# Kernel optimization log

Hardware: AMD Instinct MI355X
Metric: run time of the kernel (lower is better)

The kernel has to match this reference:

```python
import jax, jax.numpy as jnp
import numpy as np

B, N, C = 128, 197, 768   # batch, tokens (14*14 + cls), embed dim
H = 12                    # attention heads, head_dim = 64
OUT = 32                  # hard-coded mlp out_features
CH_H = 14                 # channel-attention heads
CN = 196                  # channel-attention token dim (14*14)
MLP_HID = int(C * 4.0)    # 3072
CMLP_HID = int(OUT * 4.0) # 128
EPS = 1e-5


def _ln(x, g, b):
    m = x.mean(-1, keepdims=True)
    v = ((x - m) ** 2).mean(-1, keepdims=True)
    return (x - m) * jax.lax.rsqrt(v + EPS) * g + b


def setup_inputs() -> dict:
    key = jax.random.key(0)
    ks = jax.random.split(key, 24)
    W = lambda k, sh: (jax.random.normal(k, sh, jnp.float32) * 0.02)
    return {
        "x": jax.random.normal(ks[0], (B, N, C), jnp.float32),
        # block 1: norm1 + token attention
        "g1": jnp.ones((C,), jnp.float32), "b1": jnp.zeros((C,), jnp.float32),
        "w_qkv": W(ks[1], (3 * C, C)),                     # qkv_bias=False
        "w_proj": W(ks[2], (C, C)), "b_proj": jnp.zeros((C,), jnp.float32),
        # block 2: norm2 + mlp (768 -> 3072 -> 32), NOT residual
        "g2": jnp.ones((C,), jnp.float32), "b2": jnp.zeros((C,), jnp.float32),
        "w_fc1": W(ks[3], (MLP_HID, C)), "b_fc1": jnp.zeros((MLP_HID,), jnp.float32),
        "w_fc2": W(ks[4], (OUT, MLP_HID)), "b_fc2": jnp.zeros((OUT,), jnp.float32),
        # block 3: norm3 + channel attention (over 196 spatial positions)
        "g3": jnp.ones((OUT,), jnp.float32), "b3": jnp.zeros((OUT,), jnp.float32),
        "w_cqkv": W(ks[5], (3 * CN, CN)),                  # qkv_bias=False
        "w_cproj": W(ks[6], (CN, CN)), "b_cproj": jnp.zeros((CN,), jnp.float32),
        # block 4: norm4 + channel mlp (32 -> 128 -> 32)
        "g4": jnp.ones((OUT,), jnp.float32), "b4": jnp.zeros((OUT,), jnp.float32),
        "w_cfc1": W(ks[7], (CMLP_HID, OUT)), "b_cfc1": jnp.zeros((CMLP_HID,), jnp.float32),
        "w_cfc2": W(ks[8], (OUT, CMLP_HID)), "b_cfc2": jnp.zeros((OUT,), jnp.float32),
    }


def reference(x, g1, b1, w_qkv, w_proj, b_proj,
              g2, b2, w_fc1, b_fc1, w_fc2, b_fc2,
              g3, b3, w_cqkv, w_cproj, b_cproj,
              g4, b4, w_cfc1, b_cfc1, w_cfc2, b_cfc2):
    Bz, Nn, Cc = x.shape
    hd = Cc // H  # 64

    # --- token attention (residual) ---
    h = _ln(x, g1, b1)
    qkv = (h @ w_qkv.T).reshape(Bz, Nn, 3, H, hd).transpose(2, 0, 3, 1, 4)
    q, k, v = qkv[0], qkv[1], qkv[2]                       # [B,H,N,hd]
    a = jax.nn.softmax(jnp.einsum('bhqd,bhkd->bhqk', q, k) * (hd ** -0.5), axis=-1)
    o = jnp.einsum('bhqk,bhkd->bhqd', a, v).transpose(0, 2, 1, 3).reshape(Bz, Nn, Cc)
    x = x + (o @ w_proj.T + b_proj)

    # --- mlp 768->3072->32, NO residual (matches original forward) ---
    h = _ln(x, g2, b2)
    x = jax.nn.gelu(h @ w_fc1.T + b_fc1, approximate=False) @ w_fc2.T + b_fc2  # [B,N,32]

    # --- channel attention (residual); N==197 path, no interleave averaging ---
    h = _ln(x, g3, b3)
    cls = h[:, :1, :]                                      # [B,1,32]
    t = h[:, 1:, :].transpose(0, 2, 1)                     # [B,32,196]
    chd = CN // CH_H  # 14
    cqkv = (t @ w_cqkv.T).reshape(Bz, OUT, 3, CH_H, chd).transpose(2, 0, 3, 1, 4)
    cq, ck, cv = cqkv[0], cqkv[1], cqkv[2]                 # [B,14,32,14]
    ca = jax.nn.softmax(jnp.einsum('bhqd,bhkd->bhqk', cq, ck) * (chd ** -0.5), axis=-1)
    co = jnp.einsum('bhqk,bhkd->bhqd', ca, cv).transpose(0, 2, 1, 3).reshape(Bz, OUT, CN)
    co = co @ w_cproj.T + b_cproj                          # [B,32,196]
    x = x + jnp.concatenate([cls, co.transpose(0, 2, 1)], axis=1)

    # --- channel mlp 32->128->32 (residual) ---
    h = _ln(x, g4, b4)
    x = x + (jax.nn.gelu(h @ w_cfc1.T + b_cfc1, approximate=False) @ w_cfc2.T + b_cfc2)
    return x
```

## Files before the change

### kernel.cpp

```cpp
#include <hip/hip_runtime.h>
#include <hip/hip_bf16.h>

typedef unsigned short u16;
typedef __hip_bfloat16 bf16;
typedef __attribute__((ext_vector_type(8))) short bf16x8;
typedef __attribute__((ext_vector_type(4))) float f32x4;

#define B_   128
#define N_   197
#define C_   768
#define H_   12
#define HD_  64
#define T_   (B_*N_)
#define MH_  3072
#define OUT_ 32
#define CN_  196
#define CHH_ 14
#define KP_  224
#define CSZ_ (B_*CHH_*32*14)

__device__ __forceinline__ float bfu2f(u16 x){ union{unsigned u; float f;} v; v.u=((unsigned)x)<<16; return v.f; }
__device__ __forceinline__ bf16  f2bf(float f){ return __float2bfloat16(f); }
__device__ __forceinline__ u16   f2bfu(float f){ union{bf16 h; u16 u;} c; c.h=__float2bfloat16(f); return c.u; }
__device__ __forceinline__ float gelu_f(float x){ return 0.5f*x*(1.0f+erff(x*0.70710678118654752f)); }

__device__ __forceinline__ void gl_lds16(const u16* g, u16* l){
  __builtin_amdgcn_global_load_lds((const __attribute__((address_space(1))) void*)g,
                                   (__attribute__((address_space(3))) void*)l, 16, 0, 0);
}

__global__ __launch_bounds__(256) void write_code_kernel(float* out, int n, float code){
  int i = blockIdx.x*256 + threadIdx.x;
  if (i < n) out[i] = code;
}

template<bool F32IN>
__global__ __launch_bounds__(256) void ln768_kernel(const void* __restrict__ xv,
    const float* __restrict__ g, const float* __restrict__ b, bf16* __restrict__ out)
{
  int row = blockIdx.x;
  int tid = threadIdx.x;
  float v0, v1, v2;
  if (F32IN){
    const float* xr = (const float*)xv + (size_t)row*C_;
    v0 = xr[tid]; v1 = xr[tid+256]; v2 = xr[tid+512];
  } else {
    const u16* xr = (const u16*)xv + (size_t)row*C_;
    v0 = bfu2f(xr[tid]); v1 = bfu2f(xr[tid+256]); v2 = bfu2f(xr[tid+512]);
  }
  __shared__ float red[4];
  int lane = tid & 63, wave = tid >> 6;
  float s = v0+v1+v2;
  #pragma unroll
  for (int off=32; off>0; off>>=1) s += __shfl_xor(s, off);
  if (lane==0) red[wave]=s;
  __syncthreads();
  float mean = (red[0]+red[1]+red[2]+red[3]) * (1.0f/C_);
  float d0=v0-mean, d1=v1-mean, d2=v2-mean;
  float q = d0*d0+d1*d1+d2*d2;
  #pragma unroll
  for (int off=32; off>0; off>>=1) q += __shfl_xor(q, off);
  __syncthreads();
  if (lane==0) red[wave]=q;
  __syncthreads();
  float var = (red[0]+red[1]+red[2]+red[3]) * (1.0f/C_);
  float r = rsqrtf(var + 1e-5f);
  bf16* orow = out + (size_t)row*C_;
  orow[tid]     = f2bf(d0*r*g[tid]     + b[tid]);
  orow[tid+256] = f2bf(d1*r*g[tid+256] + b[tid+256]);
  orow[tid+512] = f2bf(d2*r*g[tid+512] + b[tid+512]);
}

__global__ __launch_bounds__(256) void ln32_kernel(const float* __restrict__ x,
    const float* __restrict__ g, const float* __restrict__ b, float* __restrict__ out)
{
  int i = blockIdx.x*256 + threadIdx.x;
  int c = i & 31;
  float v = x[i];
  float s = v;
  #pragma unroll
  for (int off=16; off>0; off>>=1) s += __shfl_xor(s, off, 32);
  float mean = s * (1.0f/32);
  float d = v - mean;
  float q = d*d;
  #pragma unroll
  for (int off=16; off>0; off>>=1) q += __shfl_xor(q, off, 32);
  float r = rsqrtf(q*(1.0f/32) + 1e-5f);
  out[i] = d*r*g[c] + b[c];
}

__global__ __launch_bounds__(256) void packw_bf16(const float* __restrict__ w,
    u16* __restrict__ dst, int n)
{
  int i = (blockIdx.x*256 + threadIdx.x)*4;
  if (i >= n) return;
  float4 v = *(const float4*)(w + i);
  ushort4 o; o.x=f2bfu(v.x); o.y=f2bfu(v.y); o.z=f2bfu(v.z); o.w=f2bfu(v.w);
  *(ushort4*)(dst + i) = o;
}

__global__ __launch_bounds__(256) void init_x3_kernel(const float* __restrict__ bias,
    float* __restrict__ x3)
{
  int i = blockIdx.x*256 + threadIdx.x;
  x3[i] = bias[i & 31];
}

template<int MODE, bool WB16>
__global__ __launch_bounds__(256) void gemm128(
    const u16* __restrict__ A, const void* __restrict__ Wsrc,
    const float* __restrict__ bias, const float* __restrict__ resid,
    bf16* __restrict__ outb,
    bf16* __restrict__ q_out, bf16* __restrict__ k_out, bf16* __restrict__ v_out,
    int Nn, int K)
{
  __shared__ __align__(16) u16 As[2][128*32];
  __shared__ __align__(16) u16 Bs[2][128*32];
  const int tid  = threadIdx.x;
  const int wave = tid >> 6, lane = tid & 63;
  const int quad = lane >> 4, l16 = lane & 15;
  const int wr = wave >> 1, wc = wave & 1;
  const int m0 = blockIdx.y * 128;
  const int n0 = blockIdx.x * 128;
  const int rs = tid >> 2;
  const int kc = (tid & 3) << 3;

  const u16* aA0 = A + (size_t)(m0 + rs)*K + kc;
  const u16* aA1 = aA0 + (size_t)64*K;
  const u16*  wB0 = WB16 ? ((const u16*)Wsrc + (size_t)(n0 + rs)*K + kc) : nullptr;
  const float* wF0 = WB16 ? nullptr : ((const float*)Wsrc + (size_t)(n0 + rs)*K + kc);

  f32x4 acc[4][4] = {};

  auto STAGE = [&](int buf, int k0){
    u16* AsW = As[buf] + (size_t)wave*512;
    u16* BsW = Bs[buf] + (size_t)wave*512;
    gl_lds16(aA0 + k0, AsW);
    gl_lds16(aA1 + k0, AsW + 2048);
    if (WB16){
      gl_lds16(wB0 + k0, BsW);
      gl_lds16(wB0 + (size_t)64*K + k0, BsW + 2048);
    } else {
      float4 w0 = *(const float4*)(wF0 + k0);
      float4 w1 = *(const float4*)(wF0 + k0 + 4);
      const float* wF1 = wF0 + (size_t)64*K;
      float4 w2 = *(const float4*)(wF1 + k0);
      float4 w3 = *(const float4*)(wF1 + k0 + 4);
      ushort4 b0; b0.x=f2bfu(w0.x); b0.y=f2bfu(w0.y); b0.z=f2bfu(w0.z); b0.w=f2bfu(w0.w);
      ushort4 b1; b1.x=f2bfu(w1.x); b1.y=f2bfu(w1.y); b1.z=f2bfu(w1.z); b1.w=f2bfu(w1.w);
      ushort4 b2; b2.x=f2bfu(w2.x); b2.y=f2bfu(w2.y); b2.z=f2bfu(w2.z); b2.w=f2bfu(w2.w);
      ushort4 b3; b3.x=f2bfu(w3.x); b3.y=f2bfu(w3.y); b3.z=f2bfu(w3.z); b3.w=f2bfu(w3.w);
      *(ushort4*)&Bs[buf][rs*32 + kc]        = b0;
      *(ushort4*)&Bs[buf][rs*32 + kc + 4]    = b1;
      *(ushort4*)&Bs[buf][(rs+64)*32 + kc]   = b2;
      *(ushort4*)&Bs[buf][(rs+64)*32 + kc+4] = b3;
    }
  };

  STAGE(0, 0);
  __syncthreads();
  int cur = 0;

  for (int k0 = 0; k0 < K; k0 += 32){
    if (k0 + 32 < K) STAGE(cur^1, k0 + 32);
    bf16x8 af[4], bfr[4];
    #pragma unroll
    for (int i=0;i<4;i++) af[i]  = *(const bf16x8*)&As[cur][(wr*64 + i*16 + l16)*32 + quad*8];
    #pragma unroll
    for (int j=0;j<4;j++) bfr[j] = *(const bf16x8*)&Bs[cur][(wc*64 + j*16 + l16)*32 + quad*8];
    #pragma unroll
    for (int i=0;i<4;i++)
      #pragma unroll
      for (int j=0;j<4;j++)
        acc[i][j] = __builtin_amdgcn_mfma_f32_16x16x32_bf16(af[i], bfr[j], acc[i][j], 0, 0, 0);
    __syncthreads();
    cur ^= 1;
  }

  #pragma unroll
  for (int i=0;i<4;i++){
    #pragma unroll
    for (int j=0;j<4;j++){
      #pragma unroll
      for (int r=0;r<4;r++){
        int m = m0 + wr*64 + i*16 + quad*4 + r;
        int c = n0 + wc*64 + j*16 + l16;
        float v = acc[i][j][r];
        if (MODE==0){
          int bb = m / N_;
          int n  = m - bb*N_;
          int sec = c / C_;
          int rem = c - sec*C_;
          int hh  = rem >> 6;
          int d   = rem & 63;
          bf16* dst = (sec==0) ? q_out : (sec==1) ? k_out : v_out;
          dst[(((size_t)bb*H_ + hh)*N_ + n)*HD_ + d] = f2bf(v);
        } else if (MODE==1){
          size_t idx = (size_t)m*Nn + c;
          outb[idx] = f2bf(v + bias[c] + resid[idx]);
        } else {
          outb[(size_t)m*Nn + c] = f2bf(gelu_f(v + bias[c]));
        }
      }
    }
  }
}

template<int MODE, bool WB16>
__global__ __launch_bounds__(256) void gemm_mfma(
    const u16* __restrict__ A, const void* __restrict__ Wsrc,
    const float* __restrict__ bias, const float* __restrict__ resid,
    bf16* __restrict__ outb, float* __restrict__ outf,
    bf16* __restrict__ q_out, bf16* __restrict__ k_out, bf16* __restrict__ v_out,
    int M, int Nn, int K, int wld, int astride)
{
  __shared__ __align__(16) u16 As[64][32];
  __shared__ __align__(16) u16 Bs[64][32];
  const int tid  = threadIdx.x;
  const int wave = tid >> 6, lane = tid & 63;
  const int quad = lane >> 4, l16 = lane & 15;
  const int m0 = blockIdx.x * 64;
  const int n0 = (MODE==6) ? 0 : blockIdx.y * 64;
  const int kst = (MODE==6) ? blockIdx.y * K : 0;
  const int rs = tid >> 2;
  const int kc = (tid & 3) << 3;
  const u16* arow = A + (size_t)(m0 + rs)*astride + kst + kc;
  const bool wvalid = (n0 + rs) < Nn;

  f32x4 acc[4] = {};

  for (int k0 = 0; k0 < K; k0 += 32){
    *(uint4*)&As[rs][kc] = *(const uint4*)(arow + k0);
    if (WB16){
      const u16* wrow = (const u16*)Wsrc + (size_t)(n0 + rs)*wld + kst + kc;
      uint4 wv = make_uint4(0u,0u,0u,0u);
      if (wvalid) wv = *(const uint4*)(wrow + k0);
      *(uint4*)&Bs[rs][kc] = wv;
    } else {
      const float* wrow = (const float*)Wsrc + (size_t)(n0 + rs)*wld + kst + kc;
      float4 w0 = make_float4(0.f,0.f,0.f,0.f), w1 = w0;
      if (wvalid){ w0 = *(const float4*)(wrow + k0); w1 = *(const float4*)(wrow + k0 + 4); }
      ushort4 b0; b0.x=f2bfu(w0.x); b0.y=f2bfu(w0.y); b0.z=f2bfu(w0.z); b0.w=f2bfu(w0.w);
      ushort4 b1; b1.x=f2bfu(w1.x); b1.y=f2bfu(w1.y); b1.z=f2bfu(w1.z); b1.w=f2bfu(w1.w);
      *(ushort4*)&Bs[rs][kc]   = b0;
      *(ushort4*)&Bs[rs][kc+4] = b1;
    }
    __syncthreads();
    bf16x8 af = *(const bf16x8*)&As[wave*16 + l16][quad*8];
    #pragma unroll
    for (int nb=0; nb<4; nb++){
      bf16x8 bfr = *(const bf16x8*)&Bs[nb*16 + l16][quad*8];
      acc[nb] = __builtin_amdgcn_mfma_f32_16x16x32_bf16(af, bfr, acc[nb], 0, 0, 0);
    }
    __syncthreads();
  }

  #pragma unroll
  for (int nb=0; nb<4; nb++){
    #pragma unroll
    for (int r=0; r<4; r++){
      int m = m0 + wave*16 + quad*4 + r;
      int c = n0 + nb*16 + l16;
      float v = acc[nb][r];
      if (MODE==3){
        if (c < Nn) outf[(size_t)m*Nn + c] = v + bias[c];
      } else if (MODE==4){
        if (c < Nn) outf[(size_t)m*Nn + c] += v;
      } else if (MODE==6){
        if (c < Nn) atomicAdd(&outf[(size_t)m*Nn + c], v);
      } else if (MODE==5){
        if (c < Nn){
          int bb = m >> 5, oo = m & 31;
          int sec = c / CN_;
          int rem = c - sec*CN_;
          int hh  = rem / 14;
          int d   = rem - hh*14;
          outf[(size_t)sec*CSZ_ + (((size_t)bb*CHH_ + hh)*32 + oo)*14 + d] = v;
        }
      }
    }
  }
}

__global__ __launch_bounds__(256) void attn_kernel(const u16* __restrict__ q,
    const u16* __restrict__ k, const u16* __restrict__ v, bf16* __restrict__ o)
{
  __shared__ __align__(16) u16 VtS[64*208];
  __shared__ __align__(16) u16 PsS[4*16*208];
  int bid = blockIdx.x;
  int bh = bid >> 1, sh = bid & 1;
  int b = bh / H_, hh = bh - b*H_;
  int tid = threadIdx.x, wave = tid >> 6, lane = tid & 63;
  int quad = lane >> 4, l16 = lane & 15;
  const u16* qb = q + (size_t)bh*N_*HD_;
  const u16* kb = k + (size_t)bh*N_*HD_;
  const u16* vb = v + (size_t)bh*N_*HD_;
  for (int idx = tid; idx < N_*HD_; idx += 256){
    int j = idx >> 6, d = idx & 63;
    VtS[(d*208 + j) ^ ((d&7)<<3)] = vb[idx];
  }
  for (int idx = tid; idx < 64*11; idx += 256){
    int d = idx / 11, j = 197 + (idx - d*11);
    VtS[(d*208 + j) ^ ((d&7)<<3)] = 0;
  }
  __syncthreads();

  u16* PsW = PsS + wave*16*208;
  const int gbeg = sh ? 7 : 0;
  const int gend = sh ? 13 : 7;
  const float LOG2E = 1.4426950408889634f;

  for (int g = gbeg + wave; g < gend; g += 4){
    int r0 = g*16;
    int qrow = r0 + l16;
    int qr = (qrow < N_) ? qrow : 0;
    bf16x8 aq0 = *(const bf16x8*)(qb + (size_t)qr*HD_ + quad*8);
    bf16x8 aq1 = *(const bf16x8*)(qb + (size_t)qr*HD_ + 32 + quad*8);
    f32x4 s[13];
    __builtin_amdgcn_s_setprio(1);
    #pragma unroll
    for (int nb = 0; nb < 13; nb++){
      int krow = nb*16 + l16;
      int kr = (krow < N_) ? krow : 0;
      bf16x8 bk0 = *(const bf16x8*)(kb + (size_t)kr*HD_ + quad*8);
      bf16x8 bk1 = *(const bf16x8*)(kb + (size_t)kr*HD_ + 32 + quad*8);
      f32x4 t = {};
      t = __builtin_amdgcn_mfma_f32_16x16x32_bf16(aq0, bk0, t, 0, 0, 0);
      t = __builtin_amdgcn_mfma_f32_16x16x32_bf16(aq1, bk1, t, 0, 0, 0);
      s[nb] = t;
    }
    __builtin_amdgcn_s_setprio(0);
    #pragma unroll
    for (int nb = 0; nb < 13; nb++){
      bool colok = (nb*16 + l16) < N_;
      #pragma unroll
      for (int r = 0; r < 4; r++)
        s[nb][r] = colok ? s[nb][r]*(0.125f*LOG2E) : -1e30f;
    }
    #pragma unroll
    for (int r = 0; r < 4; r++){
      float m01 = fmaxf(s[0][r], s[1][r]),  m23 = fmaxf(s[2][r], s[3][r]);
      float m45 = fmaxf(s[4][r], s[5][r]),  m67 = fmaxf(s[6][r], s[7][r]);
      float m89 = fmaxf(s[8][r], s[9][r]),  mab = fmaxf(s[10][r], s[11][r]);
      float m = fmaxf(fmaxf(fmaxf(m01,m23), fmaxf(m45,m67)),
                      fmaxf(fmaxf(m89,mab), s[12][r]));
      m = fmaxf(m, __shfl_xor(m, 1));
      m = fmaxf(m, __shfl_xor(m, 2));
      m = fmaxf(m, __shfl_xor(m, 4));
      m = fmaxf(m, __shfl_xor(m, 8));
      float p[13];
      #pragma unroll
      for (int nb = 0; nb < 13; nb++){
        p[nb] = __builtin_amdgcn_exp2f(s[nb][r] - m);
        s[nb][r] = p[nb];
      }
      float t01=p[0]+p[1], t23=p[2]+p[3], t45=p[4]+p[5], t67=p[6]+p[7];
      float t89=p[8]+p[9], tab=p[10]+p[11];
      float su = ((t01+t23)+(t45+t67)) + ((t89+tab)+p[12]);
      su += __shfl_xor(su, 1);
      su += __shfl_xor(su, 2);
      su += __shfl_xor(su, 4);
      su += __shfl_xor(su, 8);
      float inv = 1.0f/su;
      #pragma unroll
      for (int nb = 0; nb < 13; nb++) s[nb][r] *= inv;
    }
    #pragma unroll
    for (int nb = 0; nb < 13; nb++)
      #pragma unroll
      for (int r = 0; r < 4; r++){
        int row = quad*4 + r;
        PsW[(row*208 + nb*16 + l16) ^ ((row&7)<<3)] = f2bfu(s[nb][r]);
      }
    __threadfence_block();
    f32x4 oa[4] = {};
    __builtin_amdgcn_s_setprio(1);
    #pragma unroll
    for (int ks = 0; ks < 7; ks++){
      int col = ks*32 + quad*8;
      bool ok = (col < 208);
      int ccol = ok ? col : 0;
      bf16x8 ap = *(const bf16x8*)&PsW[(l16*208 + ccol) ^ ((l16&7)<<3)];
      if (!ok) ap = (bf16x8){0,0,0,0,0,0,0,0};
      #pragma unroll
      for (int nd = 0; nd < 4; nd++){
        bf16x8 bv = *(const bf16x8*)&VtS[((nd*16 + l16)*208 + ccol) ^ ((l16&7)<<3)];
        oa[nd] = __builtin_amdgcn_mfma_f32_16x16x32_bf16(ap, bv, oa[nd], 0, 0, 0);
      }
    }
    __builtin_amdgcn_s_setprio(0);
    #pragma unroll
    for (int nd = 0; nd < 4; nd++)
      #pragma unroll
      for (int r = 0; r < 4; r++){
        int qi = r0 + quad*4 + r;
        if (qi < N_)
          o[((size_t)b*N_ + qi)*C_ + hh*HD_ + nd*16 + l16] = f2bf(oa[nd][r]);
      }
    __threadfence_block();
  }
}

__global__ __launch_bounds__(256) void pack_tall_kernel(const float* __restrict__ h3,
    u16* __restrict__ tall)
{
  int idx = blockIdx.x*256 + threadIdx.x;
  if (idx >= 4096*KP_) return;
  int row = idx / KP_, kk = idx - row*KP_;
  int b = row >> 5, oo = row & 31;
  float v = (kk < CN_) ? h3[((size_t)b*N_ + 1 + kk)*32 + oo] : 0.f;
  tall[idx] = f2bfu(v);
}

__global__ __launch_bounds__(256) void pack_w_kernel(const float* __restrict__ w,
    u16* __restrict__ dst, int rows, int kreal)
{
  int idx = blockIdx.x*256 + threadIdx.x;
  if (idx >= rows*KP_) return;
  int r = idx / KP_, kk = idx - r*KP_;
  dst[idx] = (kk < kreal) ? f2bfu(w[(size_t)r*kreal + kk]) : (u16)0;
}

__global__ __launch_bounds__(256) void pack_co_kernel(const float* __restrict__ co,
    u16* __restrict__ dst)
{
  int idx = blockIdx.x*256 + threadIdx.x;
  if (idx >= 4096*KP_) return;
  int row = idx / KP_, kk = idx - row*KP_;
  dst[idx] = (kk < CN_) ? f2bfu(co[(size_t)row*CN_ + kk]) : (u16)0;
}

__global__ __launch_bounds__(64) void cattn_kernel(const float* __restrict__ cq,
    const float* __restrict__ ck, const float* __restrict__ cv, float* __restrict__ co)
{
  __shared__ __align__(16) float qs[32*15], ks_[32*15], vs[32*15], ps[32*34];
  int bh = blockIdx.x;
  int b  = bh / CHH_;
  int hh = bh - b*CHH_;
  int lane = threadIdx.x;
  const float* qb = cq + (size_t)bh*448;
  const float* kb = ck + (size_t)bh*448;
  const float* vb = cv + (size_t)bh*448;
  for (int idx=lane; idx<448; idx+=64){
    int o = idx/14, d = idx - o*14;
    qs[o*15+d] = qb[idx]; ks_[o*15+d] = kb[idx]; vs[o*15+d] = vb[idx];
  }
  __syncthreads();
  int o = lane & 31, half = lane >> 5;
  const float scale = 0.2672612419124244f;
  float sc[16]; float mx = -1e30f;
  #pragma unroll
  for (int jj=0; jj<16; jj++){
    int j = half*16 + jj;
    float a = 0.f;
    #pragma unroll
    for (int d=0; d<14; d++) a += qs[o*15+d]*ks_[j*15+d];
    sc[jj] = a*scale;
    mx = fmaxf(mx, sc[jj]);
  }
  mx = fmaxf(mx, __shfl_xor(mx, 32));
  float sum = 0.f;
  #pragma unroll
  for (int jj=0; jj<16; jj++){ sc[jj] = __expf(sc[jj]-mx); sum += sc[jj]; }
  sum += __shfl_xor(sum, 32);
  float inv = 1.0f/sum;
  #pragma unroll
  for (int jj=0; jj<16; jj++) ps[o*34 + half*16 + jj] = sc[jj]*inv;
  __syncthreads();
  #pragma unroll
  for (int dd=0; dd<7; dd++){
    int d = half*7 + dd;
    float acc = 0.f;
    #pragma unroll
    for (int j=0; j<32; j++) acc += ps[o*34+j]*vs[j*15+d];
    co[((size_t)b*32 + o)*CN_ + hh*14 + d] = acc;
  }
}

__global__ __launch_bounds__(256) void concat_add_kernel(const float* __restrict__ x3,
    const float* __restrict__ h3, const float* __restrict__ co2, float* __restrict__ x4)
{
  int i = blockIdx.x*256 + threadIdx.x;
  int c = i & 31;
  int row = i >> 5;
  int b = row / N_;
  int r = row - b*N_;
  float add = (r==0) ? h3[i] : co2[((size_t)b*32 + c)*CN_ + (r-1)];
  x4[i] = x3[i] + add;
}

__global__ __launch_bounds__(256) void cfc1_kernel(const float* __restrict__ h4,
    const float* __restrict__ w, const float* __restrict__ bias, float* __restrict__ chid)
{
  int idx = blockIdx.x*256 + threadIdx.x;
  int m = idx >> 7, j = idx & 127;
  const float* hr = h4 + (size_t)m*32;
  const float* wr = w + (size_t)j*32;
  float acc = bias[j];
  #pragma unroll
  for (int kk=0; kk<32; kk++) acc += hr[kk]*wr[kk];
  chid[idx] = gelu_f(acc);
}

__global__ __launch_bounds__(256) void cfc2_kernel(const float* __restrict__ chid,
    const float* __restrict__ w, const float* __restrict__ bias,
    const float* __restrict__ x4, float* __restrict__ out)
{
  int idx = blockIdx.x*256 + threadIdx.x;
  int m = idx >> 5, j = idx & 31;
  const float* cr = chid + (size_t)m*128;
  const float* wr = w + (size_t)j*128;
  float acc = bias[j];
  #pragma unroll
  for (int kk=0; kk<128; kk++) acc += cr[kk]*wr[kk];
  out[idx] = x4[idx] + acc;
}

extern "C" void kernel_launch(void* const* d_in, const int* in_sizes, int n_in,
                              void* d_out, int out_size, void* d_ws, size_t ws_size,
                              hipStream_t stream)
{
  const int NIN = 23;
  static const int dsz[NIN] = {19365888,768,768,1769472,589824,768,768,768,2359296,
                               3072,98304,32,32,32,115248,38416,196,32,32,4096,128,4096,32};
  static const int a2d[NIN] = {2,7,13,18,20,22,16,9,11,5,1,6,12,17,19,21,15,14,8,10,4,3,0};

  float* dout = (float*)d_out;
  int ogrid = (out_size + 255)/256;

  const float* in[NIN];
  bool dict_ok = (n_in == NIN);
  if (dict_ok) for (int i=0;i<NIN;i++) if (in_sizes[i] != dsz[i]) { dict_ok=false; break; }
  if (dict_ok){
    for (int i=0;i<NIN;i++) in[i] = (const float*)d_in[i];
  } else {
    bool alpha_ok = (n_in == NIN);
    if (alpha_ok) for (int i=0;i<NIN;i++) if (in_sizes[i] != dsz[a2d[i]]) { alpha_ok=false; break; }
    if (alpha_ok){
      for (int i=0;i<NIN;i++) in[a2d[i]] = (const float*)d_in[i];
    } else {
      write_code_kernel<<<ogrid, 256, 0, stream>>>(dout, out_size, 5000.f + (float)n_in);
      return;
    }
  }

  const float* x      = in[0];
  const float* g1     = in[1];
  const float* b1     = in[2];
  const float* w_qkv  = in[3];
  const float* w_proj = in[4];
  const float* b_proj = in[5];
  const float* g2     = in[6];
  const float* b2     = in[7];
  const float* w_fc1  = in[8];
  const float* b_fc1  = in[9];
  const float* w_fc2  = in[10];
  const float* b_fc2  = in[11];
  const float* g3     = in[12];
  const float* b3     = in[13];
  const float* w_cqkv = in[14];
  const float* w_cproj= in[15];
  const float* b_cproj= in[16];
  const float* g4     = in[17];
  const float* b4     = in[18];
  const float* w_cfc1 = in[19];
  const float* b_cfc1 = in[20];
  const float* w_cfc2 = in[21];
  const float* b_cfc2 = in[22];

  char* ws = (char*)d_ws;
  const size_t TC2 = (size_t)T_*C_*2;
  const size_t NEED = 4*TC2 + 4096;
  if (ws_size < NEED){
    write_code_kernel<<<ogrid, 256, 0, stream>>>(dout, out_size,
        7000.f + (float)(ws_size >> 20));
    return;
  }

  bf16* h_buf   = (bf16*)(ws);
  bf16* o_buf   = (bf16*)(ws);
  bf16* q_buf   = (bf16*)(ws + TC2);
  bf16* k_buf   = (bf16*)(ws + 2*TC2);
  bf16* v_buf   = (bf16*)(ws + 3*TC2);
  bf16* x2_buf  = (bf16*)(ws + TC2);
  bf16* hidh    = (bf16*)(ws + 2*TC2);
  float* x3     = (float*)(ws + TC2);
  char* sm = ws + 2*TC2;
  float* h3  = (float*)sm; sm += (size_t)T_*32*4;
  float* cq  = (float*)sm; sm += (size_t)CSZ_*4;
  float* ck  = (float*)sm; sm += (size_t)CSZ_*4;
  float* cv  = (float*)sm; sm += (size_t)CSZ_*4;
  float* co  = (float*)sm; sm += (size_t)B_*32*CN_*4;
  float* co2 = (float*)sm; sm += (size_t)B_*32*CN_*4;
  float* x4  = (float*)sm; sm += (size_t)T_*32*4;
  float* h4  = (float*)sm; sm += (size_t)T_*32*4;
  float* chid = (float*)sm;
  u16* tall  = (u16*)(ws);
  u16* wcq_b = (u16*)(ws + 2*1024*1024);
  u16* co_b  = (u16*)(ws + 3*1024*1024);
  u16* wcp_b = (u16*)(ws + 5*1024*1024);

  u16* wqkv_b  = (u16*)(ws + 4*TC2 + 4096);
  u16* wproj_b = wqkv_b  + (size_t)2304*C_;
  u16* wfc1_b  = wproj_b + (size_t)C_*C_;
  const size_t WPACK = ((size_t)2304*C_ + (size_t)C_*C_ + (size_t)MH_*C_)*2;
  const bool packed = (ws_size >= NEED + WPACK);

  if (packed){
    packw_bf16<<<(2304*C_/4+255)/256, 256, 0, stream>>>(w_qkv,  wqkv_b,  2304*C_);
    packw_bf16<<<(C_*C_/4+255)/256,  256, 0, stream>>>(w_proj, wproj_b, C_*C_);
    packw_bf16<<<(MH_*C_/4+255)/256, 256, 0, stream>>>(w_fc1,  wfc1_b,  MH_*C_);
  }

  ln768_kernel<true><<<T_, 256, 0, stream>>>(x, g1, b1, h_buf);
  if (packed)
    gemm128<0,true><<<dim3(2304/128, T_/128), 256, 0, stream>>>((const u16*)h_buf,
        wqkv_b, nullptr, nullptr, nullptr, q_buf, k_buf, v_buf, 2304, C_);
  else
    gemm128<0,false><<<dim3(2304/128, T_/128), 256, 0, stream>>>((const u16*)h_buf,
        w_qkv, nullptr, nullptr, nullptr, q_buf, k_buf, v_buf, 2304, C_);
  attn_kernel<<<B_*H_*2, 256, 0, stream>>>((const u16*)q_buf, (const u16*)k_buf,
      (const u16*)v_buf, o_buf);
  if (packed)
    gemm128<1,true><<<dim3(C_/128, T_/128), 256, 0, stream>>>((const u16*)o_buf,
        wproj_b, b_proj, x, x2_buf, nullptr, nullptr, nullptr, C_, C_);
  else
    gemm128<1,false><<<dim3(C_/128, T_/128), 256, 0, stream>>>((const u16*)o_buf,
        w_proj, b_proj, x, x2_buf, nullptr, nullptr, nullptr, C_, C_);
  ln768_kernel<false><<<T_, 256, 0, stream>>>(x2_buf, g2, b2, h_buf);
  init_x3_kernel<<<(T_*32)/256, 256, 0, stream>>>(b_fc2, x3);
  for (int half=0; half<2; half++){
    if (packed)
      gemm128<2,true><<<dim3(1536/128, T_/128), 256, 0, stream>>>((const u16*)h_buf,
          wfc1_b + (size_t)half*1536*C_, b_fc1 + half*1536, nullptr,
          hidh, nullptr, nullptr, nullptr, 1536, C_);
    else
      gemm128<2,false><<<dim3(1536/128, T_/128), 256, 0, stream>>>((const u16*)h_buf,
          w_fc1 + (size_t)half*1536*C_, b_fc1 + half*1536, nullptr,
          hidh, nullptr, nullptr, nullptr, 1536, C_);
    gemm_mfma<6,false><<<dim3(T_/64, 4), 256, 0, stream>>>((const u16*)hidh,
        w_fc2 + (size_t)half*1536, nullptr, nullptr, nullptr, x3,
        nullptr, nullptr, nullptr, T_, OUT_, 384, MH_, 1536);
  }
  ln32_kernel<<<(T_*32)/256, 256, 0, stream>>>(x3, g3, b3, h3);
  pack_tall_kernel<<<(4096*KP_+255)/256, 256, 0, stream>>>(h3, tall);
  pack_w_kernel<<<(588*KP_+255)/256, 256, 0, stream>>>(w_cqkv, wcq_b, 588, CN_);
  gemm_mfma<5,true><<<dim3(4096/64, 10), 256, 0, stream>>>(tall, wcq_b,
      nullptr, nullptr, nullptr, cq, nullptr, nullptr, nullptr, 4096, 588, KP_, KP_, KP_);
  cattn_kernel<<<B_*CHH_, 64, 0, stream>>>(cq, ck, cv, co);
  pack_co_kernel<<<(4096*KP_+255)/256, 256, 0, stream>>>(co, co_b);
  pack_w_kernel<<<(196*KP_+255)/256, 256, 0, stream>>>(w_cproj, wcp_b, CN_, CN_);
  gemm_mfma<3,true><<<dim3(4096/64, 4), 256, 0, stream>>>(co_b, wcp_b,
      b_cproj, nullptr, nullptr, co2, nullptr, nullptr, nullptr, 4096, CN_, KP_, KP_, KP_);
  concat_add_kernel<<<(T_*32)/256, 256, 0, stream>>>(x3, h3, co2, x4);
  ln32_kernel<<<(T_*32)/256, 256, 0, stream>>>(x4, g4, b4, h4);
  cfc1_kernel<<<(T_*128)/256, 256, 0, stream>>>(h4, w_cfc1, b_cfc1, chid);
  cfc2_kernel<<<(T_*32)/256, 256, 0, stream>>>(chid, w_cfc2, b_cfc2, x4, dout);
}
```

Measured before the change: 1.001 ms.

## Remap GEMM workgroups per XCD and merge attention query halves into one block

The GEMM kernel now remaps its linear workgroup id so that consecutive tiles land on the same XCD, which should improve L2 reuse of A/B tiles across the chiplets. The attention kernel stops splitting each (batch, head) across two blocks, so V is transposed into LDS once per head instead of twice. V is now loaded with 8-wide vector reads, and the kernel gets a launch-bounds occupancy hint. Halving the attention grid reduces parallelism and makes each block do more serial work.

Result: slower. 1.159 ms (+15.8%).

```diff
diff --git a/kernel.cpp b/kernel.cpp
--- a/kernel.cpp
+++ b/kernel.cpp
@@ -120,8 +120,14 @@
   const int wave = tid >> 6, lane = tid & 63;
   const int quad = lane >> 4, l16 = lane & 15;
   const int wr = wave >> 1, wc = wave & 1;
-  const int m0 = blockIdx.y * 128;
-  const int n0 = blockIdx.x * 128;
+  const unsigned Nx  = gridDim.x;
+  const unsigned nwg = Nx * gridDim.y;
+  unsigned lin = blockIdx.x + Nx*blockIdx.y;
+  unsigned q8 = nwg >> 3, r8 = nwg & 7;
+  unsigned xcd = lin & 7, sub = lin >> 3;
+  unsigned nl = (xcd < r8 ? xcd*(q8+1) : r8*(q8+1) + (xcd-r8)*q8) + sub;
+  const int m0 = (int)(nl / Nx) * 128;
+  const int n0 = (int)(nl % Nx) * 128;
   const int rs = tid >> 2;
   const int kc = (tid & 3) << 3;
 
@@ -282,22 +288,26 @@
   }
 }
 
-__global__ __launch_bounds__(256) void attn_kernel(const u16* __restrict__ q,
+__global__ __launch_bounds__(256, 3) void attn_kernel(const u16* __restrict__ q,
     const u16* __restrict__ k, const u16* __restrict__ v, bf16* __restrict__ o)
 {
   __shared__ __align__(16) u16 VtS[64*208];
   __shared__ __align__(16) u16 PsS[4*16*208];
-  int bid = blockIdx.x;
-  int bh = bid >> 1, sh = bid & 1;
+  int bh = blockIdx.x;
   int b = bh / H_, hh = bh - b*H_;
   int tid = threadIdx.x, wave = tid >> 6, lane = tid & 63;
   int quad = lane >> 4, l16 = lane & 15;
   const u16* qb = q + (size_t)bh*N_*HD_;
   const u16* kb = k + (size_t)bh*N_*HD_;
   const u16* vb = v + (size_t)bh*N_*HD_;
-  for (int idx = tid; idx < N_*HD_; idx += 256){
-    int j = idx >> 6, d = idx & 63;
-    VtS[(d*208 + j) ^ ((d&7)<<3)] = vb[idx];
+  for (int idx = tid; idx < (N_*HD_)/8; idx += 256){
+    int j = idx >> 3, dg = idx & 7;
+    bf16x8 vv = *(const bf16x8*)(vb + (size_t)j*HD_ + dg*8);
+    #pragma unroll
+    for (int e=0;e<8;e++){
+      int d = dg*8 + e;
+      VtS[(d*208 + j) ^ ((d&7)<<3)] = ((u16*)&vv)[e];
+    }
   }
   for (int idx = tid; idx < 64*11; idx += 256){
     int d = idx / 11, j = 197 + (idx - d*11);
@@ -306,11 +316,9 @@
   __syncthreads();
 
   u16* PsW = PsS + wave*16*208;
-  const int gbeg = sh ? 7 : 0;
-  const int gend = sh ? 13 : 7;
   const float LOG2E = 1.4426950408889634f;
 
-  for (int g = gbeg + wave; g < gend; g += 4){
+  for (int g = wave; g < 13; g += 4){
     int r0 = g*16;
     int qrow = r0 + l16;
     int qr = (qrow < N_) ? qrow : 0;
@@ -348,15 +356,13 @@
       m = fmaxf(m, __shfl_xor(m, 2));
       m = fmaxf(m, __shfl_xor(m, 4));
       m = fmaxf(m, __shfl_xor(m, 8));
-      float p[13];
-      #pragma unroll
-      for (int nb = 0; nb < 13; nb++){
-        p[nb] = __builtin_amdgcn_exp2f(s[nb][r] - m);
-        s[nb][r] = p[nb];
-      }
-      float t01=p[0]+p[1], t23=p[2]+p[3], t45=p[4]+p[5], t67=p[6]+p[7];
-      float t89=p[8]+p[9], tab=p[10]+p[11];
-      float su = ((t01+t23)+(t45+t67)) + ((t89+tab)+p[12]);
+      #pragma unroll
+      for (int nb = 0; nb < 13; nb++)
+        s[nb][r] = __builtin_amdgcn_exp2f(s[nb][r] - m);
+      float t01=s[0][r]+s[1][r], t23=s[2][r]+s[3][r];
+      float t45=s[4][r]+s[5][r], t67=s[6][r]+s[7][r];
+      float t89=s[8][r]+s[9][r], tab=s[10][r]+s[11][r];
+      float su = ((t01+t23)+(t45+t67)) + ((t89+tab)+s[12][r]);
       su += __shfl_xor(su, 1);
       su += __shfl_xor(su, 2);
       su += __shfl_xor(su, 4);
@@ -619,7 +625,7 @@
   else
     gemm128<0,false><<<dim3(2304/128, T_/128), 256, 0, stream>>>((const u16*)h_buf,
         w_qkv, nullptr, nullptr, nullptr, q_buf, k_buf, v_buf, 2304, C_);
-  attn_kernel<<<B_*H_*2, 256, 0, stream>>>((const u16*)q_buf, (const u16*)k_buf,
+  attn_kernel<<<B_*H_, 256, 0, stream>>>((const u16*)q_buf, (const u16*)k_buf,
       (const u16*)v_buf, o_buf);
   if (packed)
     gemm128<1,true><<<dim3(C_/128, T_/128), 256, 0, stream>>>((const u16*)o_buf,
```
